# Kernel tuning notes

Measured on AMD Instinct MI355X. Metric: run time of the kernel, lower is better.

## Reference

```python
import jax, jax.numpy as jnp
import numpy as np

FP4_LUT = jnp.array([0.0, 0.5, 1.0, 1.5, 2.0, 3.0, 4.0, 6.0], dtype=jnp.float32)
BLOCK = 16  # NVFP4 block size along in-features


def dequant_nvfp4(packed, scale, gscale):
    """packed: [K//2, N] int32 bytes (two fp4 e2m1 codes, lo nibble = even in-feature);
    scale: [K//16, N] block scales; gscale: scalar global scale.
    Returns W^T laid out [K, N] (in_features, out_features)."""
    lo = packed & 0xF
    hi = (packed >> 4) & 0xF
    codes = jnp.stack([lo, hi], axis=1).reshape(-1, packed.shape[1])  # [K, N]
    vals = jnp.where(codes >= 8, -1.0, 1.0) * FP4_LUT[codes & 7]
    K, N = vals.shape
    vals = (vals.reshape(K // BLOCK, BLOCK, N) * scale[:, None, :]).reshape(K, N)
    return vals * gscale


def setup_inputs() -> dict:
    key = jax.random.key(0)
    ks = jax.random.split(key, 6)
    E, H, I, T = 8, 2048, 4096, 1024
    hidden_states = jax.random.normal(ks[0], (E * T, H), dtype=jnp.float32)
    gate_up_packed = jax.random.randint(ks[1], (E, H // 2, 2 * I), 0, 256, dtype=jnp.int32)
    down_packed = jax.random.randint(ks[2], (E, I // 2, H), 0, 256, dtype=jnp.int32)
    # block scales: positive, e4m3-representable magnitudes
    gate_up_scale = (0.5 + jax.random.uniform(ks[3], (E, H // 16, 2 * I))) * 0.05
    down_scale = (0.5 + jax.random.uniform(ks[4], (E, I // 16, H))) * 0.05
    gate_up_gscale = jnp.float32(0.5)
    down_gscale = jnp.float32(0.5)
    return {"hidden_states": hidden_states, "gate_up_packed": gate_up_packed,
            "gate_up_scale": gate_up_scale, "gate_up_gscale": gate_up_gscale,
            "down_packed": down_packed, "down_scale": down_scale,
            "down_gscale": down_gscale}


def reference(hidden_states, gate_up_packed, gate_up_scale, gate_up_gscale,
              down_packed, down_scale, down_gscale):
    E = gate_up_packed.shape[0]
    H = hidden_states.shape[-1]
    x = hidden_states.reshape(E, -1, H)  # [E, T, H], tokens contiguous per expert

    def body(_, inp):
        xe, gup, gus, dp, ds = inp
        Wgu = dequant_nvfp4(gup, gus, gate_up_gscale)  # [H, 2I]
        Wd = dequant_nvfp4(dp, ds, down_gscale)        # [I, H]
        gu = xe @ Wgu                                   # [T, 2I]
        gate, up = jnp.split(gu, 2, axis=-1)
        inter = up * jax.nn.silu(gate)
        return None, inter @ Wd                         # [T, H]

    _, out = jax.lax.scan(body, None,
                          (x, gate_up_packed, gate_up_scale, down_packed, down_scale))
    return out.reshape(-1, H)
```

## Files before the change

kernel.cpp:

```cpp
#include <hip/hip_runtime.h>
#include <stdint.h>

#define E_ 8
#define H_ 2048
#define I_ 4096
#define T_ 1024
#define N1_ (2 * I_)

typedef unsigned short ushort_t;
typedef __attribute__((ext_vector_type(8))) __bf16 bf16x8;
typedef __attribute__((ext_vector_type(4))) float f32x4;

__device__ __forceinline__ ushort_t f2bf(float f) {
    return (ushort_t)((__float_as_uint(f) + 0x8000u) >> 16);
}
__device__ __forceinline__ uint32_t pk2bf(float a, float b) {
    uint32_t ua = __float_as_uint(a) + 0x8000u;
    uint32_t ub = __float_as_uint(b) + 0x8000u;
    return __builtin_amdgcn_perm(ub, ua, 0x07060302u);
}

__device__ __forceinline__ uint32_t dq_pair(uint32_t w, float s) {
    const uint32_t LO_HI = 0xC0804000u, LO_LO = 0xC0800000u;
    const uint32_t HI_HI = 0x40404040u, HI_LO = 0x3F3F3F00u;
    uint32_t sel = (w & 0x7u) | ((w & 0x70u) << 4);
    uint32_t lo  = __builtin_amdgcn_perm(LO_HI, LO_LO, sel);
    uint32_t hi  = __builtin_amdgcn_perm(HI_HI, HI_LO, sel);
    uint32_t pair = __builtin_amdgcn_perm(hi, lo, 0x05010400u);
    pair |= ((w & 8u) << 12) | ((w & 0x80u) << 24);
    uint32_t b0 = __float_as_uint(__uint_as_float(pair << 16) * s) + 0x8000u;
    uint32_t b1 = __float_as_uint(__uint_as_float(pair & 0xFFFF0000u) * s) + 0x8000u;
    return __builtin_amdgcn_perm(b1, b0, 0x07060302u);
}

__global__ __launch_bounds__(512, 4) void gemm1_kernel(
    const float* __restrict__ x,
    const int* __restrict__ gup,
    const float* __restrict__ gus,
    const float* __restrict__ gscale_p,
    ushort_t* __restrict__ inter,
    int e0) {
    __shared__ __align__(16) ushort_t As[256 * 40];
    __shared__ __align__(16) ushort_t Bs[128 * 40];

    const int tid = threadIdx.x;
    const int lane = tid & 63, wv = tid >> 6;
    const int quad = lane >> 4, c16 = lane & 15;
    const int mw = wv >> 1, nw = wv & 1;
    const int zloc = blockIdx.z, e = e0 + zloc;
    const int mBase = blockIdx.y * 256, nTile = blockIdx.x;
    const float gsc = gscale_p[0];

    const int bn = tid & 127, kq = tid >> 7;
    const int colg = nTile * 64 + (bn & 63) + ((bn >> 6) << 12);
    const int* bptr = gup + (size_t)e * (H_ / 2) * N1_ + (size_t)(kq * 4) * N1_ + colg;
    const float* sptr = gus + (size_t)e * (H_ / 16) * N1_ + (size_t)(kq >> 1) * N1_ + colg;
    uint4* bs_w = (uint4*)(&Bs[bn * 40 + kq * 8]);

    const int arow = tid >> 3, seg = tid & 7;
    const float* ap = x + (size_t)(e * T_ + mBase + arow) * H_ + seg * 4;

    f32x4 accg[4][2], accu[4][2];
    const f32x4 z4 = {0.f, 0.f, 0.f, 0.f};
#pragma unroll
    for (int f = 0; f < 4; ++f)
#pragma unroll
        for (int b = 0; b < 2; ++b) { accg[f][b] = z4; accu[f][b] = z4; }

    for (int kt = 0; kt < H_ / 32; ++kt) {
        float4 fa[4];
#pragma unroll
        for (int p = 0; p < 4; ++p)
            fa[p] = *(const float4*)(ap + (size_t)(p * 64) * H_ + kt * 32);
        int wt[4];
#pragma unroll
        for (int i = 0; i < 4; ++i) wt[i] = bptr[(size_t)i * N1_];
        float s = sptr[0] * gsc;

#pragma unroll
        for (int p = 0; p < 4; ++p) {
            uint2 d;
            d.x = pk2bf(fa[p].x, fa[p].y);
            d.y = pk2bf(fa[p].z, fa[p].w);
            *(uint2*)(&As[(arow + p * 64) * 40 + seg * 4]) = d;
        }
        uint4 q;
        q.x = dq_pair((uint32_t)wt[0], s); q.y = dq_pair((uint32_t)wt[1], s);
        q.z = dq_pair((uint32_t)wt[2], s); q.w = dq_pair((uint32_t)wt[3], s);
        *bs_w = q;

        bptr += (size_t)16 * N1_;
        sptr += (size_t)2 * N1_;
        __syncthreads();

        bf16x8 bg0 = *(const bf16x8*)(&Bs[(nw * 32 + c16) * 40 + quad * 8]);
        bf16x8 bg1 = *(const bf16x8*)(&Bs[(nw * 32 + 16 + c16) * 40 + quad * 8]);
        bf16x8 bu0 = *(const bf16x8*)(&Bs[(64 + nw * 32 + c16) * 40 + quad * 8]);
        bf16x8 bu1 = *(const bf16x8*)(&Bs[(64 + nw * 32 + 16 + c16) * 40 + quad * 8]);
#pragma unroll
        for (int f = 0; f < 4; ++f) {
            bf16x8 af = *(const bf16x8*)(&As[(mw * 64 + f * 16 + c16) * 40 + quad * 8]);
            accg[f][0] = __builtin_amdgcn_mfma_f32_16x16x32_bf16(af, bg0, accg[f][0], 0, 0, 0);
            accg[f][1] = __builtin_amdgcn_mfma_f32_16x16x32_bf16(af, bg1, accg[f][1], 0, 0, 0);
            accu[f][0] = __builtin_amdgcn_mfma_f32_16x16x32_bf16(af, bu0, accu[f][0], 0, 0, 0);
            accu[f][1] = __builtin_amdgcn_mfma_f32_16x16x32_bf16(af, bu1, accu[f][1], 0, 0, 0);
        }
        __syncthreads();
    }

    ushort_t* ip = inter + (size_t)zloc * T_ * I_;
#pragma unroll
    for (int f = 0; f < 4; ++f)
#pragma unroll
        for (int b = 0; b < 2; ++b)
#pragma unroll
            for (int r = 0; r < 4; ++r) {
                int row = mBase + mw * 64 + f * 16 + quad * 4 + r;
                int col = nTile * 64 + nw * 32 + b * 16 + c16;
                float g = accg[f][b][r];
                float u = accu[f][b][r];
                float v = u * g / (1.f + __expf(-g));
                ip[(size_t)row * I_ + col] = f2bf(v);
            }
}

__global__ __launch_bounds__(512, 4) void gemm2_kernel(
    const ushort_t* __restrict__ inter,
    const int* __restrict__ dp,
    const float* __restrict__ dsc,
    const float* __restrict__ gscale_p,
    float* __restrict__ out,
    int e0) {
    __shared__ __align__(16) ushort_t As[256 * 40];
    __shared__ __align__(16) ushort_t Bs[128 * 40];

    const int tid = threadIdx.x;
    const int lane = tid & 63, wv = tid >> 6;
    const int quad = lane >> 4, c16 = lane & 15;
    const int mw = wv >> 1, nw = wv & 1;
    const int zloc = blockIdx.z, e = e0 + zloc;
    const int mBase = blockIdx.y * 256, nBase = blockIdx.x * 128;
    const float gsc = gscale_p[0];

    const int bn = tid & 127, kq = tid >> 7;
    const int col = nBase + bn;
    const int* bptr = dp + (size_t)e * (I_ / 2) * H_ + (size_t)(kq * 4) * H_ + col;
    const float* sptr = dsc + (size_t)e * (I_ / 16) * H_ + (size_t)(kq >> 1) * H_ + col;
    uint4* bs_w = (uint4*)(&Bs[bn * 40 + kq * 8]);

    const int arow = tid >> 2, seg = tid & 3;
    const ushort_t* ap = inter + (size_t)(zloc * T_ + mBase + arow) * I_ + seg * 8;

    f32x4 acc[4][4];
    const f32x4 z4 = {0.f, 0.f, 0.f, 0.f};
#pragma unroll
    for (int f = 0; f < 4; ++f)
#pragma unroll
        for (int b = 0; b < 4; ++b) acc[f][b] = z4;

    for (int kt = 0; kt < I_ / 32; ++kt) {
        uint4 va[2];
#pragma unroll
        for (int p = 0; p < 2; ++p)
            va[p] = *(const uint4*)(ap + (size_t)(p * 128) * I_ + kt * 32);
        int wt[4];
#pragma unroll
        for (int i = 0; i < 4; ++i) wt[i] = bptr[(size_t)i * H_];
        float s = sptr[0] * gsc;

#pragma unroll
        for (int p = 0; p < 2; ++p)
            *(uint4*)(&As[(arow + p * 128) * 40 + seg * 8]) = va[p];
        uint4 q;
        q.x = dq_pair((uint32_t)wt[0], s); q.y = dq_pair((uint32_t)wt[1], s);
        q.z = dq_pair((uint32_t)wt[2], s); q.w = dq_pair((uint32_t)wt[3], s);
        *bs_w = q;

        bptr += (size_t)16 * H_;
        sptr += (size_t)2 * H_;
        __syncthreads();

        bf16x8 bfr[4];
#pragma unroll
        for (int b = 0; b < 4; ++b)
            bfr[b] = *(const bf16x8*)(&Bs[(nw * 64 + b * 16 + c16) * 40 + quad * 8]);
#pragma unroll
        for (int f = 0; f < 4; ++f) {
            bf16x8 af = *(const bf16x8*)(&As[(mw * 64 + f * 16 + c16) * 40 + quad * 8]);
#pragma unroll
            for (int b = 0; b < 4; ++b)
                acc[f][b] = __builtin_amdgcn_mfma_f32_16x16x32_bf16(af, bfr[b], acc[f][b], 0, 0, 0);
        }
        __syncthreads();
    }

#pragma unroll
    for (int f = 0; f < 4; ++f)
#pragma unroll
        for (int b = 0; b < 4; ++b)
#pragma unroll
            for (int r = 0; r < 4; ++r) {
                int row = mBase + mw * 64 + f * 16 + quad * 4 + r;
                int c = nBase + nw * 64 + b * 16 + c16;
                out[(size_t)(e * T_ + row) * H_ + c] = acc[f][b][r];
            }
}

extern "C" void kernel_launch(void* const* d_in, const int* in_sizes, int n_in,
                              void* d_out, int out_size, void* d_ws, size_t ws_size,
                              hipStream_t stream) {
    const float* x = (const float*)d_in[0];
    const int* gup = (const int*)d_in[1];
    const float* gus = (const float*)d_in[2];
    const float* gug = (const float*)d_in[3];
    const int* dp = (const int*)d_in[4];
    const float* dsc = (const float*)d_in[5];
    const float* dg = (const float*)d_in[6];
    float* out = (float*)d_out;
    ushort_t* inter = (ushort_t*)d_ws;

    const size_t per_e = (size_t)T_ * I_ * 2;
    int C = 8;
    if (ws_size < 8 * per_e) C = (ws_size >= 4 * per_e) ? 4 : (ws_size >= 2 * per_e) ? 2 : 1;

    for (int e0 = 0; e0 < E_; e0 += C) {
        gemm1_kernel<<<dim3(I_ / 64, T_ / 256, C), 512, 0, stream>>>(x, gup, gus, gug, inter, e0);
        gemm2_kernel<<<dim3(H_ / 128, T_ / 256, C), 512, 0, stream>>>(inter, dp, dsc, dg, out, e0);
    }
}
```

Before: 1.023 ms.

## Double-buffer LDS tiles and prefetch next k-tile in both GEMM kernels

Both GEMM kernels now use two LDS buffers for A and B tiles. The global loads for the next k-step are issued before the MFMA work on the current tile, and the converted data is written into the alternate buffer afterwards, so only one barrier per iteration is needed. This is meant to hide global-load and dequantization latency behind matrix math. It doubles LDS use per block, which can cut the number of resident blocks per CU and increases register pressure.

```diff
diff --git a/kernel.cpp b/kernel.cpp
--- a/kernel.cpp
+++ b/kernel.cpp
@@ -40,8 +40,8 @@
     const float* __restrict__ gscale_p,
     ushort_t* __restrict__ inter,
     int e0) {
-    __shared__ __align__(16) ushort_t As[256 * 40];
-    __shared__ __align__(16) ushort_t Bs[128 * 40];
+    __shared__ __align__(16) ushort_t As[2][256 * 40];
+    __shared__ __align__(16) ushort_t Bs[2][128 * 40];
 
     const int tid = threadIdx.x;
     const int lane = tid & 63, wv = tid >> 6;
@@ -55,7 +55,6 @@
     const int colg = nTile * 64 + (bn & 63) + ((bn >> 6) << 12);
     const int* bptr = gup + (size_t)e * (H_ / 2) * N1_ + (size_t)(kq * 4) * N1_ + colg;
     const float* sptr = gus + (size_t)e * (H_ / 16) * N1_ + (size_t)(kq >> 1) * N1_ + colg;
-    uint4* bs_w = (uint4*)(&Bs[bn * 40 + kq * 8]);
 
     const int arow = tid >> 3, seg = tid & 7;
     const float* ap = x + (size_t)(e * T_ + mBase + arow) * H_ + seg * 4;
@@ -67,45 +66,74 @@
 #pragma unroll
         for (int b = 0; b < 2; ++b) { accg[f][b] = z4; accu[f][b] = z4; }
 
-    for (int kt = 0; kt < H_ / 32; ++kt) {
-        float4 fa[4];
+    float4 fa[4]; int wt[4]; float sv;
+#pragma unroll
+    for (int p = 0; p < 4; ++p) fa[p] = *(const float4*)(ap + (size_t)(p * 64) * H_);
+#pragma unroll
+    for (int i = 0; i < 4; ++i) wt[i] = bptr[(size_t)i * N1_];
+    sv = sptr[0] * gsc;
+    {
+#pragma unroll
+        for (int p = 0; p < 4; ++p) {
+            uint2 d; d.x = pk2bf(fa[p].x, fa[p].y); d.y = pk2bf(fa[p].z, fa[p].w);
+            *(uint2*)(&As[0][(arow + p * 64) * 40 + seg * 4]) = d;
+        }
+        uint4 q;
+        q.x = dq_pair((uint32_t)wt[0], sv); q.y = dq_pair((uint32_t)wt[1], sv);
+        q.z = dq_pair((uint32_t)wt[2], sv); q.w = dq_pair((uint32_t)wt[3], sv);
+        *(uint4*)(&Bs[0][bn * 40 + kq * 8]) = q;
+    }
+    __syncthreads();
+
+    for (int kt = 0; kt < H_ / 32 - 1; ++kt) {
+        const int cur = kt & 1, nxt = cur ^ 1;
 #pragma unroll
         for (int p = 0; p < 4; ++p)
-            fa[p] = *(const float4*)(ap + (size_t)(p * 64) * H_ + kt * 32);
-        int wt[4];
-#pragma unroll
-        for (int i = 0; i < 4; ++i) wt[i] = bptr[(size_t)i * N1_];
-        float s = sptr[0] * gsc;
-
-#pragma unroll
-        for (int p = 0; p < 4; ++p) {
-            uint2 d;
-            d.x = pk2bf(fa[p].x, fa[p].y);
-            d.y = pk2bf(fa[p].z, fa[p].w);
-            *(uint2*)(&As[(arow + p * 64) * 40 + seg * 4]) = d;
-        }
-        uint4 q;
-        q.x = dq_pair((uint32_t)wt[0], s); q.y = dq_pair((uint32_t)wt[1], s);
-        q.z = dq_pair((uint32_t)wt[2], s); q.w = dq_pair((uint32_t)wt[3], s);
-        *bs_w = q;
-
-        bptr += (size_t)16 * N1_;
-        sptr += (size_t)2 * N1_;
-        __syncthreads();
-
-        bf16x8 bg0 = *(const bf16x8*)(&Bs[(nw * 32 + c16) * 40 + quad * 8]);
-        bf16x8 bg1 = *(const bf16x8*)(&Bs[(nw * 32 + 16 + c16) * 40 + quad * 8]);
-        bf16x8 bu0 = *(const bf16x8*)(&Bs[(64 + nw * 32 + c16) * 40 + quad * 8]);
-        bf16x8 bu1 = *(const bf16x8*)(&Bs[(64 + nw * 32 + 16 + c16) * 40 + quad * 8]);
-#pragma unroll
-        for (int f = 0; f < 4; ++f) {
-            bf16x8 af = *(const bf16x8*)(&As[(mw * 64 + f * 16 + c16) * 40 + quad * 8]);
+            fa[p] = *(const float4*)(ap + (size_t)(p * 64) * H_ + (kt + 1) * 32);
+        const int* bp = bptr + (size_t)(kt + 1) * 16 * N1_;
+#pragma unroll
+        for (int i = 0; i < 4; ++i) wt[i] = bp[(size_t)i * N1_];
+        sv = sptr[(size_t)(kt + 1) * 2 * N1_] * gsc;
+
+        bf16x8 bg0 = *(const bf16x8*)(&Bs[cur][(nw * 32 + c16) * 40 + quad * 8]);
+        bf16x8 bg1 = *(const bf16x8*)(&Bs[cur][(nw * 32 + 16 + c16) * 40 + quad * 8]);
+        bf16x8 bu0 = *(const bf16x8*)(&Bs[cur][(64 + nw * 32 + c16) * 40 + quad * 8]);
+        bf16x8 bu1 = *(const bf16x8*)(&Bs[cur][(64 + nw * 32 + 16 + c16) * 40 + quad * 8]);
+#pragma unroll
+        for (int f = 0; f < 4; ++f) {
+            bf16x8 af = *(const bf16x8*)(&As[cur][(mw * 64 + f * 16 + c16) * 40 + quad * 8]);
             accg[f][0] = __builtin_amdgcn_mfma_f32_16x16x32_bf16(af, bg0, accg[f][0], 0, 0, 0);
             accg[f][1] = __builtin_amdgcn_mfma_f32_16x16x32_bf16(af, bg1, accg[f][1], 0, 0, 0);
             accu[f][0] = __builtin_amdgcn_mfma_f32_16x16x32_bf16(af, bu0, accu[f][0], 0, 0, 0);
             accu[f][1] = __builtin_amdgcn_mfma_f32_16x16x32_bf16(af, bu1, accu[f][1], 0, 0, 0);
         }
+
+#pragma unroll
+        for (int p = 0; p < 4; ++p) {
+            uint2 d; d.x = pk2bf(fa[p].x, fa[p].y); d.y = pk2bf(fa[p].z, fa[p].w);
+            *(uint2*)(&As[nxt][(arow + p * 64) * 40 + seg * 4]) = d;
+        }
+        uint4 q;
+        q.x = dq_pair((uint32_t)wt[0], sv); q.y = dq_pair((uint32_t)wt[1], sv);
+        q.z = dq_pair((uint32_t)wt[2], sv); q.w = dq_pair((uint32_t)wt[3], sv);
+        *(uint4*)(&Bs[nxt][bn * 40 + kq * 8]) = q;
         __syncthreads();
+    }
+
+    {
+        const int cur = (H_ / 32 - 1) & 1;
+        bf16x8 bg0 = *(const bf16x8*)(&Bs[cur][(nw * 32 + c16) * 40 + quad * 8]);
+        bf16x8 bg1 = *(const bf16x8*)(&Bs[cur][(nw * 32 + 16 + c16) * 40 + quad * 8]);
+        bf16x8 bu0 = *(const bf16x8*)(&Bs[cur][(64 + nw * 32 + c16) * 40 + quad * 8]);
+        bf16x8 bu1 = *(const bf16x8*)(&Bs[cur][(64 + nw * 32 + 16 + c16) * 40 + quad * 8]);
+#pragma unroll
+        for (int f = 0; f < 4; ++f) {
+            bf16x8 af = *(const bf16x8*)(&As[cur][(mw * 64 + f * 16 + c16) * 40 + quad * 8]);
+            accg[f][0] = __builtin_amdgcn_mfma_f32_16x16x32_bf16(af, bg0, accg[f][0], 0, 0, 0);
+            accg[f][1] = __builtin_amdgcn_mfma_f32_16x16x32_bf16(af, bg1, accg[f][1], 0, 0, 0);
+            accu[f][0] = __builtin_amdgcn_mfma_f32_16x16x32_bf16(af, bu0, accu[f][0], 0, 0, 0);
+            accu[f][1] = __builtin_amdgcn_mfma_f32_16x16x32_bf16(af, bu1, accu[f][1], 0, 0, 0);
+        }
     }
 
     ushort_t* ip = inter + (size_t)zloc * T_ * I_;
@@ -131,8 +159,8 @@
     const float* __restrict__ gscale_p,
     float* __restrict__ out,
     int e0) {
-    __shared__ __align__(16) ushort_t As[256 * 40];
-    __shared__ __align__(16) ushort_t Bs[128 * 40];
+    __shared__ __align__(16) ushort_t As[2][256 * 40];
+    __shared__ __align__(16) ushort_t Bs[2][128 * 40];
 
     const int tid = threadIdx.x;
     const int lane = tid & 63, wv = tid >> 6;
@@ -146,7 +174,6 @@
     const int col = nBase + bn;
     const int* bptr = dp + (size_t)e * (I_ / 2) * H_ + (size_t)(kq * 4) * H_ + col;
     const float* sptr = dsc + (size_t)e * (I_ / 16) * H_ + (size_t)(kq >> 1) * H_ + col;
-    uint4* bs_w = (uint4*)(&Bs[bn * 40 + kq * 8]);
 
     const int arow = tid >> 2, seg = tid & 3;
     const ushort_t* ap = inter + (size_t)(zloc * T_ + mBase + arow) * I_ + seg * 8;
@@ -158,40 +185,68 @@
 #pragma unroll
         for (int b = 0; b < 4; ++b) acc[f][b] = z4;
 
-    for (int kt = 0; kt < I_ / 32; ++kt) {
-        uint4 va[2];
+    uint4 va[2]; int wt[4]; float sv;
+#pragma unroll
+    for (int p = 0; p < 2; ++p) va[p] = *(const uint4*)(ap + (size_t)(p * 128) * I_);
+#pragma unroll
+    for (int i = 0; i < 4; ++i) wt[i] = bptr[(size_t)i * H_];
+    sv = sptr[0] * gsc;
+    {
 #pragma unroll
         for (int p = 0; p < 2; ++p)
-            va[p] = *(const uint4*)(ap + (size_t)(p * 128) * I_ + kt * 32);
-        int wt[4];
-#pragma unroll
-        for (int i = 0; i < 4; ++i) wt[i] = bptr[(size_t)i * H_];
-        float s = sptr[0] * gsc;
-
+            *(uint4*)(&As[0][(arow + p * 128) * 40 + seg * 8]) = va[p];
+        uint4 q;
+        q.x = dq_pair((uint32_t)wt[0], sv); q.y = dq_pair((uint32_t)wt[1], sv);
+        q.z = dq_pair((uint32_t)wt[2], sv); q.w = dq_pair((uint32_t)wt[3], sv);
+        *(uint4*)(&Bs[0][bn * 40 + kq * 8]) = q;
+    }
+    __syncthreads();
+
+    for (int kt = 0; kt < I_ / 32 - 1; ++kt) {
+        const int cur = kt & 1, nxt = cur ^ 1;
 #pragma unroll
         for (int p = 0; p < 2; ++p)
-            *(uint4*)(&As[(arow + p * 128) * 40 + seg * 8]) = va[p];
-        uint4 q;
-        q.x = dq_pair((uint32_t)wt[0], s); q.y = dq_pair((uint32_t)wt[1], s);
-        q.z = dq_pair((uint32_t)wt[2], s); q.w = dq_pair((uint32_t)wt[3], s);
-        *bs_w = q;
-
-        bptr += (size_t)16 * H_;
-        sptr += (size_t)2 * H_;
-        __syncthreads();
+            va[p] = *(const uint4*)(ap + (size_t)(p * 128) * I_ + (kt + 1) * 32);
+        const int* bp = bptr + (size_t)(kt + 1) * 16 * H_;
+#pragma unroll
+        for (int i = 0; i < 4; ++i) wt[i] = bp[(size_t)i * H_];
+        sv = sptr[(size_t)(kt + 1) * 2 * H_] * gsc;
 
         bf16x8 bfr[4];
 #pragma unroll
         for (int b = 0; b < 4; ++b)
-            bfr[b] = *(const bf16x8*)(&Bs[(nw * 64 + b * 16 + c16) * 40 + quad * 8]);
-#pragma unroll
-        for (int f = 0; f < 4; ++f) {
-            bf16x8 af = *(const bf16x8*)(&As[(mw * 64 + f * 16 + c16) * 40 + quad * 8]);
+            bfr[b] = *(const bf16x8*)(&Bs[cur][(nw * 64 + b * 16 + c16) * 40 + quad * 8]);
+#pragma unroll
+        for (int f = 0; f < 4; ++f) {
+            bf16x8 af = *(const bf16x8*)(&As[cur][(mw * 64 + f * 16 + c16) * 40 + quad * 8]);
 #pragma unroll
             for (int b = 0; b < 4; ++b)
                 acc[f][b] = __builtin_amdgcn_mfma_f32_16x16x32_bf16(af, bfr[b], acc[f][b], 0, 0, 0);
         }
+
+#pragma unroll
+        for (int p = 0; p < 2; ++p)
+            *(uint4*)(&As[nxt][(arow + p * 128) * 40 + seg * 8]) = va[p];
+        uint4 q;
+        q.x = dq_pair((uint32_t)wt[0], sv); q.y = dq_pair((uint32_t)wt[1], sv);
+        q.z = dq_pair((uint32_t)wt[2], sv); q.w = dq_pair((uint32_t)wt[3], sv);
+        *(uint4*)(&Bs[nxt][bn * 40 + kq * 8]) = q;
         __syncthreads();
+    }
+
+    {
+        const int cur = (I_ / 32 - 1) & 1;
+        bf16x8 bfr[4];
+#pragma unroll
+        for (int b = 0; b < 4; ++b)
+            bfr[b] = *(const bf16x8*)(&Bs[cur][(nw * 64 + b * 16 + c16) * 40 + quad * 8]);
+#pragma unroll
+        for (int f = 0; f < 4; ++f) {
+            bf16x8 af = *(const bf16x8*)(&As[cur][(mw * 64 + f * 16 + c16) * 40 + quad * 8]);
+#pragma unroll
+            for (int b = 0; b < 4; ++b)
+                acc[f][b] = __builtin_amdgcn_mfma_f32_16x16x32_bf16(af, bfr[b], acc[f][b], 0, 0, 0);
+        }
     }
 
 #pragma unroll
```

Result: no change. 1.020 ms (-0.3%).
